# Kernel optimization log

Hardware: AMD Instinct MI355X
Metric: run time of the kernel (lower is better)

## Reference

```python
import jax, jax.numpy as jnp
import numpy as np

V_THRESHOLD = 1.0
DETACH_RESET = True


def setup_inputs() -> dict:
    key = jax.random.key(0)
    x_seq = jax.random.normal(key, (16, 32, 128, 32, 32), dtype=jnp.float32)
    return {"x_seq": x_seq}


def reference(x_seq):
    # Multi-step integrate-and-fire: v accumulates input, emits spike when
    # v >= threshold, then soft-resets by subtracting threshold.
    th = jnp.asarray(V_THRESHOLD, dtype=x_seq.dtype)

    def step(v, x_t):
        v = v + x_t
        spike = (v >= th).astype(x_seq.dtype)
        v = v - spike * th
        if DETACH_RESET:
            v = jax.lax.stop_gradient(v)
        return v, spike

    v0 = jnp.zeros(x_seq.shape[1:], dtype=x_seq.dtype)  # (B, C, H, W)
    _, spike_seq = jax.lax.scan(step, v0, x_seq)  # (T, B, C, H, W)
    return spike_seq
```

## Files before the change

### kernel.cpp

```cpp
#include <hip/hip_runtime.h>


#define T_STEPS 16

typedef float f32x4 __attribute__((ext_vector_type(4)));

__global__ __launch_bounds__(256) void if_scan_kernel(
    const f32x4* __restrict__ x, f32x4* __restrict__ out, int n4) {
    int i = blockIdx.x * blockDim.x + threadIdx.x;
    if (i >= n4) return;

    f32x4 xv[T_STEPS];
#pragma unroll
    for (int t = 0; t < T_STEPS; ++t) {
        xv[t] = x[(size_t)t * (size_t)n4 + (size_t)i];
    }

#pragma unroll
    for (int t = 0; t < T_STEPS; ++t) {
        asm volatile("" : "+v"(xv[t]));
    }

    f32x4 v = (f32x4)(0.f);
#pragma unroll
    for (int t = 0; t < T_STEPS; ++t) {
        v += xv[t];
        f32x4 s;
        s.x = (v.x >= 1.0f) ? 1.0f : 0.0f;
        s.y = (v.y >= 1.0f) ? 1.0f : 0.0f;
        s.z = (v.z >= 1.0f) ? 1.0f : 0.0f;
        s.w = (v.w >= 1.0f) ? 1.0f : 0.0f;
        v -= s;
        __builtin_nontemporal_store(s, &out[(size_t)t * (size_t)n4 + (size_t)i]);
    }
}

extern "C" void kernel_launch(void* const* d_in, const int* in_sizes, int n_in,
                              void* d_out, int out_size, void* d_ws, size_t ws_size,
                              hipStream_t stream) {
    const float* x = (const float*)d_in[0];
    float* out = (float*)d_out;

    int total = in_sizes[0];
    int per_step = total / T_STEPS;
    int n4 = per_step / 4;

    dim3 block(256);
    dim3 grid((n4 + block.x - 1) / block.x);
    if_scan_kernel<<<grid, block, 0, stream>>>(
        (const f32x4*)x, (f32x4*)out, n4);
}
```

Before: 491.5 us.

## Process four vectors per thread per timestep instead of preloading all timesteps

Each thread now handles four float4 columns strided by 256, keeping four running potentials, and loads and stores them one timestep at a time. This replaces the earlier pattern of preloading all sixteen timesteps into registers behind an asm barrier. The grid shrinks by a factor of four and the bounds check is removed, which assumes n4 is a multiple of 1024. That holds for the test shape but would break on other shapes. Fewer loads are in flight per timestep than with the full preload, which could reduce memory-level parallelism.

```diff
diff --git a/kernel.cpp b/kernel.cpp
--- a/kernel.cpp
+++ b/kernel.cpp
@@ -2,36 +2,43 @@
 
 
 #define T_STEPS 16
+#define K_ELEMS 4
 
 typedef float f32x4 __attribute__((ext_vector_type(4)));
 
 __global__ __launch_bounds__(256) void if_scan_kernel(
     const f32x4* __restrict__ x, f32x4* __restrict__ out, int n4) {
-    int i = blockIdx.x * blockDim.x + threadIdx.x;
-    if (i >= n4) return;
+    int base = blockIdx.x * (blockDim.x * K_ELEMS) + threadIdx.x;
 
-    f32x4 xv[T_STEPS];
+    f32x4 v[K_ELEMS];
 #pragma unroll
-    for (int t = 0; t < T_STEPS; ++t) {
-        xv[t] = x[(size_t)t * (size_t)n4 + (size_t)i];
-    }
+    for (int k = 0; k < K_ELEMS; ++k) v[k] = (f32x4)(0.f);
 
 #pragma unroll
     for (int t = 0; t < T_STEPS; ++t) {
-        asm volatile("" : "+v"(xv[t]));
-    }
+        size_t off = (size_t)t * (size_t)n4 + (size_t)base;
 
-    f32x4 v = (f32x4)(0.f);
+        f32x4 a[K_ELEMS];
 #pragma unroll
-    for (int t = 0; t < T_STEPS; ++t) {
-        v += xv[t];
-        f32x4 s;
-        s.x = (v.x >= 1.0f) ? 1.0f : 0.0f;
-        s.y = (v.y >= 1.0f) ? 1.0f : 0.0f;
-        s.z = (v.z >= 1.0f) ? 1.0f : 0.0f;
-        s.w = (v.w >= 1.0f) ? 1.0f : 0.0f;
-        v -= s;
-        __builtin_nontemporal_store(s, &out[(size_t)t * (size_t)n4 + (size_t)i]);
+        for (int k = 0; k < K_ELEMS; ++k) {
+            a[k] = x[off + (size_t)(k * 256)];
+        }
+
+        f32x4 s[K_ELEMS];
+#pragma unroll
+        for (int k = 0; k < K_ELEMS; ++k) {
+            v[k] += a[k];
+            s[k].x = (v[k].x >= 1.0f) ? 1.0f : 0.0f;
+            s[k].y = (v[k].y >= 1.0f) ? 1.0f : 0.0f;
+            s[k].z = (v[k].z >= 1.0f) ? 1.0f : 0.0f;
+            s[k].w = (v[k].w >= 1.0f) ? 1.0f : 0.0f;
+            v[k] -= s[k];
+        }
+
+#pragma unroll
+        for (int k = 0; k < K_ELEMS; ++k) {
+            __builtin_nontemporal_store(s[k], &out[off + (size_t)(k * 256)]);
+        }
     }
 }
 
@@ -46,7 +53,7 @@
     int n4 = per_step / 4;
 
     dim3 block(256);
-    dim3 grid((n4 + block.x - 1) / block.x);
+    dim3 grid(n4 / (block.x * K_ELEMS));
     if_scan_kernel<<<grid, block, 0, stream>>>(
         (const f32x4*)x, (f32x4*)out, n4);
 }
```

New measurement: 442.7 us. -9.9%, faster.
